# Kernel tuning notes

Hardware: AMD Instinct MI355X
Metric: run time of the kernel (lower is better)

## Reference

```python
import jax, jax.numpy as jnp
import numpy as np

# Multi-scale deformable attention (Deformable-DETR / MMCV MSDA), faithful math.
SHAPES = [(100, 100), (50, 50), (25, 25), (13, 13)]  # (H_l, W_l) per level
B, C, NH, L, P = 2, 256, 8, 4, 4
LV = sum(h * w for h, w in SHAPES)  # 13294
LQ = LV
D = C // NH  # head dim = 32


def setup_inputs() -> dict:
    k = jax.random.split(jax.random.key(0), 10)
    rn = lambda i, sh, sc=1.0: jax.random.normal(k[i], sh, jnp.float32) * sc
    starts = np.cumsum([0] + [h * w for h, w in SHAPES])[:L]
    return {
        "query": rn(0, (LQ, B, C)),
        "reference_points": jax.random.uniform(k[1], (B, LQ, L, 2), jnp.float32),
        "value": rn(2, (LV, B, C)),
        "spatial_shapes": jnp.array(SHAPES, jnp.int32),
        "level_start_index": jnp.array(starts, jnp.int32),
        "Wv": rn(3, (C, C), C ** -0.5), "bv": jnp.zeros((C,), jnp.float32),
        "Woff": rn(4, (C, NH * L * P * 2), 0.01), "boff": rn(5, (NH * L * P * 2,), 0.3),
        "Wattn": rn(6, (C, NH * L * P), 0.02), "battn": jnp.zeros((NH * L * P,), jnp.float32),
        "Wo": rn(7, (C, C), C ** -0.5), "bo": jnp.zeros((C,), jnp.float32),
    }


def _bilinear(v, loc, Hl, Wl):
    """v: [B,NH,Hl*Wl,D]; loc: [B,Lq,NH,P,2] normalized (x,y) in (0,1).
    grid_sample(align_corners=False, padding_mode='zeros') equivalent."""
    x = loc[..., 0] * Wl - 0.5
    y = loc[..., 1] * Hl - 0.5
    x0 = jnp.floor(x); y0 = jnp.floor(y)
    wx = x - x0; wy = y - y0
    x0i = x0.astype(jnp.int32); y0i = y0.astype(jnp.int32)
    lq = loc.shape[1]
    acc = jnp.zeros((B, NH, lq * P, D), v.dtype)
    for dy, wyc in ((0, 1.0 - wy), (1, wy)):
        for dx, wxc in ((0, 1.0 - wx), (1, wx)):
            xi = x0i + dx; yi = y0i + dy
            valid = (xi >= 0) & (xi < Wl) & (yi >= 0) & (yi < Hl)
            idx = jnp.clip(yi, 0, Hl - 1) * Wl + jnp.clip(xi, 0, Wl - 1)  # [B,Lq,NH,P]
            idx2 = jnp.transpose(idx, (0, 2, 1, 3)).reshape(B, NH, lq * P)
            g = jnp.take_along_axis(v, idx2[..., None], axis=2)  # [B,NH,Lq*P,D]
            w = jnp.where(valid, wyc * wxc, 0.0).astype(v.dtype)
            w2 = jnp.transpose(w, (0, 2, 1, 3)).reshape(B, NH, lq * P, 1)
            acc = acc + g * w2
    return acc.reshape(B, NH, lq, P, D)


def _msda(q, rp, v, spatial_shapes, Wv, bv, Woff, boff, Wattn, battn, Wo, bo):
    # q: [B,Lq,C], v: [B,Lv,C] (batch-first), rp: [B,Lq,L,2]
    rp = jnp.clip(rp, 1e-5, 1.0 - 1e-5)  # wrapper clamp
    val = (v @ Wv + bv).reshape(B, LV, NH, D)
    val = jnp.transpose(val, (0, 2, 1, 3))  # [B,NH,Lv,D]
    off = (q @ Woff + boff).reshape(B, LQ, NH, L, P, 2)
    attn = jax.nn.softmax((q @ Wattn + battn).reshape(B, LQ, NH, L * P), axis=-1)
    attn = attn.reshape(B, LQ, NH, L, P)
    ss = spatial_shapes.astype(jnp.float32)
    norm = jnp.stack([ss[:, 1], ss[:, 0]], -1)  # [L,2] = (W_l, H_l)
    loc = rp[:, :, None, :, None, :] + off / norm[None, None, None, :, None, :]
    out = jnp.zeros((B, LQ, NH, D), q.dtype)
    start = 0
    for lvl, (Hl, Wl) in enumerate(SHAPES):
        vl = val[:, :, start:start + Hl * Wl]  # [B,NH,Hl*Wl,D]
        sampled = _bilinear(vl, loc[:, :, :, lvl], Hl, Wl)  # [B,NH,Lq,P,D]
        out = out + jnp.einsum('bhqpd,bqhp->bqhd', sampled, attn[:, :, :, lvl])
        start += Hl * Wl
    out = out.reshape(B, LQ, C) @ Wo + bo
    return out + q  # MMCV residual: dropout(output) + identity (dropout=0 at eval)


def reference(query, reference_points, value, spatial_shapes, level_start_index,
              Wv, bv, Woff, boff, Wattn, battn, Wo, bo):
    q = jnp.swapaxes(query, 0, 1)   # wrapper: seq-first -> batch-first
    v = jnp.swapaxes(value, 0, 1)
    out = _msda(q, reference_points, v, spatial_shapes,
                Wv, bv, Woff, boff, Wattn, battn, Wo, bo)
    return jnp.swapaxes(out, 0, 1)  # back to [Lq,B,C]
```

## Files before the change

kernel.cpp:

```cpp
#include <hip/hip_runtime.h>
#include <math.h>

namespace {

typedef __attribute__((ext_vector_type(8))) short short8;
typedef __attribute__((ext_vector_type(4))) float f32x4;
typedef __attribute__((ext_vector_type(2))) float f32x2;

constexpr int B  = 2;
constexpr int C  = 256;
constexpr int NH = 8;
constexpr int L  = 4;
constexpr int P  = 4;
constexpr int D  = 32;
constexpr int LV = 13294;
constexpr int LQ = 13294;
constexpr int M  = B * LQ;

constexpr int SZ[4]    = {100, 50, 25, 13};
constexpr int START[4] = {0, 10000, 12500, 13125};

__device__ inline short bf16r(float f) {
  unsigned u = __float_as_uint(f);
  u += 0x7fff + ((u >> 16) & 1);
  return (short)(u >> 16);
}

__device__ inline short8 cvt8(const f32x4 lo, const f32x4 hi) {
  union { uint4 u; short8 s; } r;
  asm("v_cvt_pk_bf16_f32 %0, %1, %2" : "=v"(r.u.x) : "v"(lo[0]), "v"(lo[1]));
  asm("v_cvt_pk_bf16_f32 %0, %1, %2" : "=v"(r.u.y) : "v"(lo[2]), "v"(lo[3]));
  asm("v_cvt_pk_bf16_f32 %0, %1, %2" : "=v"(r.u.z) : "v"(hi[0]), "v"(hi[1]));
  asm("v_cvt_pk_bf16_f32 %0, %1, %2" : "=v"(r.u.w) : "v"(hi[2]), "v"(hi[3]));
  return r.s;
}

__device__ inline void load_a_cvt(const float* __restrict__ arow, short8 a[8]) {
#pragma unroll
  for (int s = 0; s < 8; ++s) {
    const f32x4 lo = *reinterpret_cast<const f32x4*>(arow + s * 32);
    const f32x4 hi = *reinterpret_cast<const f32x4*>(arow + s * 32 + 4);
    a[s] = cvt8(lo, hi);
  }
}

__device__ inline void load_a_bf16(const unsigned short* __restrict__ arow, short8 a[8]) {
#pragma unroll
  for (int s = 0; s < 8; ++s)
    a[s] = *reinterpret_cast<const short8*>(arow + s * 32);
}

__device__ inline void glds16(const unsigned short* g, unsigned short* l) {
  __builtin_amdgcn_global_load_lds(
      (const __attribute__((address_space(1))) void*)g,
      (__attribute__((address_space(3))) void*)l, 16, 0, 0);
}

__global__ __launch_bounds__(256) void k_pre(
    const float* __restrict__ Wv, const float* __restrict__ Woff,
    const float* __restrict__ Wattn, const float* __restrict__ Wo,
    unsigned short* __restrict__ Btv, unsigned short* __restrict__ Btoa,
    unsigned short* __restrict__ Bto) {
  __shared__ float tile[32][33];
  const int blk = blockIdx.x;
  const float* src; unsigned short* dst; int N, local;
  if (blk < 64)       { src = Wv;    dst = Btv;              N = 256; local = blk; }
  else if (blk < 128) { src = Woff;  dst = Btoa;             N = 256; local = blk - 64; }
  else if (blk < 160) { src = Wattn; dst = Btoa + 256 * 256; N = 128; local = blk - 128; }
  else                { src = Wo;    dst = Bto;              N = 256; local = blk - 160; }
  const int ntiles = N >> 5;
  const int kt = local / ntiles, nt = local - kt * ntiles;
  const int k0 = kt << 5, n0 = nt << 5;
  const int tx = threadIdx.x & 31, ty = threadIdx.x >> 5;
#pragma unroll
  for (int r = 0; r < 4; ++r) {
    const int kk = ty + r * 8;
    tile[kk][tx] = src[(size_t)(k0 + kk) * N + n0 + tx];
  }
  __syncthreads();
#pragma unroll
  for (int r = 0; r < 4; ++r) {
    const int nn = ty + r * 8;
    const int n = n0 + nn, k = k0 + tx;
    dst[(size_t)n * 256 + (k ^ ((n & 7) << 3))] = (unsigned short)bf16r(tile[tx][nn]);
  }
}

__global__ __launch_bounds__(256, 4) void k_gemm12(
    const float* __restrict__ query, const float* __restrict__ value,
    const float* __restrict__ rp,
    const unsigned short* __restrict__ Btv, const unsigned short* __restrict__ Btoa,
    const float* __restrict__ bv, const float* __restrict__ boff,
    const float* __restrict__ battn,
    unsigned short* __restrict__ val, float* __restrict__ loc,
    float* __restrict__ attn) {
  __shared__ unsigned short sB[64 * 256];
  __shared__ float sRP[64][9];
  const int tid = threadIdx.x;
  const int wave = tid >> 6, lane = tid & 63, quad = lane >> 4, lo = lane & 15;
  const bool isval = (blockIdx.y == 0);
  const float* __restrict__ Af = isval ? value : query;
  const unsigned short* Bt  = isval ? Btv : Btoa;
  const int NC = isval ? 4 : 6;
  const int m0 = blockIdx.x * 64;
  const int mrow = m0 + wave * 16;

  short8 a[8];
  {
    const int mr = min(mrow + lo, M - 1);
    const int bb = mr / LQ, ii = mr - bb * LQ;
    load_a_cvt(Af + ((size_t)(ii * 2 + bb)) * 256 + quad * 8, a);
  }

  if (!isval && tid < 128) {
    const int r = tid >> 1, q4 = (tid & 1) * 4;
    const int mr = min(m0 + r, M - 1);
    f32x4 v = *reinterpret_cast<const f32x4*>(rp + (size_t)mr * 8 + q4);
#pragma unroll
    for (int j = 0; j < 4; ++j) v[j] = fminf(fmaxf(v[j], 1e-5f), 1.f - 1e-5f);
    *reinterpret_cast<f32x4*>(&sRP[r][q4]) = v;
  }

  const int sw = lo & 7;

#pragma unroll 1
  for (int ch = 0; ch < NC; ++ch) {
    const int n0 = ch * 64;
    __syncthreads();
    {
      const unsigned short* gsrc = Bt + (size_t)n0 * 256 + wave * 4096 + lane * 8;
      unsigned short* lbase = &sB[wave * 4096];
#pragma unroll
      for (int i = 0; i < 8; ++i)
        glds16(gsrc + i * 512, lbase + i * 512);
    }
    __syncthreads();

#pragma unroll 1
    for (int tt = 0; tt < 4; ++tt) {
      const unsigned short* bbase = &sB[(tt * 16 + lo) * 256];
      short8 b[8];
#pragma unroll
      for (int s = 0; s < 8; ++s)
        b[s] = *reinterpret_cast<const short8*>(bbase + (((quad + s * 4) ^ sw) << 3));
      f32x4 acc = (f32x4){0.f, 0.f, 0.f, 0.f};
#pragma unroll
      for (int s = 0; s < 8; ++s)
        acc = __builtin_amdgcn_mfma_f32_16x16x32_bf16(b[s], a[s], acc, 0, 0, 0);

      const int nb = n0 + tt * 16 + quad * 4;
      const int m = mrow + lo;
      if (isval) {
        const f32x4 bias4 = *reinterpret_cast<const f32x4*>(bv + nb);
        const int h = nb >> 5, d0 = nb & 31;
        if (m < M) {
          const int bb = m / LV, i = m - bb * LV;
          ushort4 o;
          o.x = (unsigned short)bf16r(acc[0] + bias4[0]);
          o.y = (unsigned short)bf16r(acc[1] + bias4[1]);
          o.z = (unsigned short)bf16r(acc[2] + bias4[2]);
          o.w = (unsigned short)bf16r(acc[3] + bias4[3]);
          *reinterpret_cast<ushort4*>(
              val + (((size_t)(bb * NH + h)) * LV + i) * D + d0) = o;
        }
      } else if (ch < 4) {
        const f32x4 bias4 = *reinterpret_cast<const f32x4*>(boff + nb);
        const int l = (nb >> 3) & 3;
        const float rsz = (l == 0) ? 0.01f : (l == 1) ? 0.02f
                        : (l == 2) ? 0.04f : (1.f / 13.f);
        if (m < M) {
          const int lr = wave * 16 + lo;
          const float rx = sRP[lr][l * 2];
          const float ry = sRP[lr][l * 2 + 1];
          f32x4 o;
          o[0] = fmaf(acc[0] + bias4[0], rsz, rx);
          o[1] = fmaf(acc[1] + bias4[1], rsz, ry);
          o[2] = fmaf(acc[2] + bias4[2], rsz, rx);
          o[3] = fmaf(acc[3] + bias4[3], rsz, ry);
          *reinterpret_cast<f32x4*>(loc + (size_t)m * 256 + nb) = o;
        }
      } else {
        const int n2 = nb - 256;
        const f32x4 bias4 = *reinterpret_cast<const f32x4*>(battn + n2);
        float v0 = acc[0] + bias4[0], v1 = acc[1] + bias4[1];
        float v2 = acc[2] + bias4[2], v3 = acc[3] + bias4[3];
        float mx = fmaxf(fmaxf(v0, v1), fmaxf(v2, v3));
        mx = fmaxf(mx, __shfl_xor(mx, 16, 64));
        mx = fmaxf(mx, __shfl_xor(mx, 32, 64));
        const float e0 = __expf(v0 - mx), e1 = __expf(v1 - mx);
        const float e2 = __expf(v2 - mx), e3 = __expf(v3 - mx);
        float s = e0 + e1 + e2 + e3;
        s += __shfl_xor(s, 16, 64);
        s += __shfl_xor(s, 32, 64);
        const float inv = 1.f / s;
        if (m < M) {
          f32x4 o; o[0] = e0 * inv; o[1] = e1 * inv; o[2] = e2 * inv; o[3] = e3 * inv;
          *reinterpret_cast<f32x4*>(attn + (size_t)m * 128 + n2) = o;
        }
      }
    }
  }
}

__global__ __launch_bounds__(256, 4) void k_gemm3(
    const unsigned short* __restrict__ tmp, const float* __restrict__ query,
    const unsigned short* __restrict__ Bt, const float* __restrict__ bo,
    float* __restrict__ out) {
  __shared__ unsigned short sB[64 * 256];
  const int tid = threadIdx.x;
  const int wave = tid >> 6, lane = tid & 63, quad = lane >> 4, lo = lane & 15;
  const int m0 = blockIdx.x * 64;
  const int mrow = m0 + wave * 16;

  short8 a[8];
  {
    const int mr = min(mrow + lo, M - 1);
    load_a_bf16(tmp + (size_t)mr * 256 + quad * 8, a);
  }
  const int sw = lo & 7;

#pragma unroll 1
  for (int ch = 0; ch < 4; ++ch) {
    const int n0 = ch * 64;
    __syncthreads();
    {
      const unsigned short* gsrc = Bt + (size_t)n0 * 256 + wave * 4096 + lane * 8;
      unsigned short* lbase = &sB[wave * 4096];
#pragma unroll
      for (int i = 0; i < 8; ++i)
        glds16(gsrc + i * 512, lbase + i * 512);
    }
    __syncthreads();

#pragma unroll 1
    for (int tt = 0; tt < 4; ++tt) {
      const unsigned short* bbase = &sB[(tt * 16 + lo) * 256];
      short8 b[8];
#pragma unroll
      for (int s = 0; s < 8; ++s)
        b[s] = *reinterpret_cast<const short8*>(bbase + (((quad + s * 4) ^ sw) << 3));
      f32x4 acc = (f32x4){0.f, 0.f, 0.f, 0.f};
#pragma unroll
      for (int s = 0; s < 8; ++s)
        acc = __builtin_amdgcn_mfma_f32_16x16x32_bf16(b[s], a[s], acc, 0, 0, 0);
      const int nb = n0 + tt * 16 + quad * 4;
      const f32x4 bias4 = *reinterpret_cast<const f32x4*>(bo + nb);
      const int m = mrow + lo;
      if (m < M) {
        const int bb = m / LQ, q = m - bb * LQ;
        const size_t o = ((size_t)(q * B + bb)) * C + nb;
        const f32x4 qv = *reinterpret_cast<const f32x4*>(query + o);
        f32x4 ov;
        ov[0] = acc[0] + bias4[0] + qv[0];
        ov[1] = acc[1] + bias4[1] + qv[1];
        ov[2] = acc[2] + bias4[2] + qv[2];
        ov[3] = acc[3] + bias4[3] + qv[3];
        *reinterpret_cast<f32x4*>(out + o) = ov;
      }
    }
  }
}

#define QB_I(v, PAT) __builtin_amdgcn_ds_swizzle((v), (PAT))
#define QB_F(v, PAT) __int_as_float(__builtin_amdgcn_ds_swizzle(__float_as_int(v), (PAT)))

__device__ inline void msda_corner(f32x2 acc[4], const uint4 r, const float w) {
  const f32x2 wv = {w, w};
  f32x2 v;
  v[0] = __uint_as_float(r.x << 16);
  v[1] = __uint_as_float(r.x & 0xffff0000u);
  acc[0] = __builtin_elementwise_fma(v, wv, acc[0]);
  v[0] = __uint_as_float(r.y << 16);
  v[1] = __uint_as_float(r.y & 0xffff0000u);
  acc[1] = __builtin_elementwise_fma(v, wv, acc[1]);
  v[0] = __uint_as_float(r.z << 16);
  v[1] = __uint_as_float(r.z & 0xffff0000u);
  acc[2] = __builtin_elementwise_fma(v, wv, acc[2]);
  v[0] = __uint_as_float(r.w << 16);
  v[1] = __uint_as_float(r.w & 0xffff0000u);
  acc[3] = __builtin_elementwise_fma(v, wv, acc[3]);
}

__global__ __launch_bounds__(256, 4) void k_sample(
    const unsigned short* __restrict__ val, const float* __restrict__ loc,
    const float* __restrict__ attn, unsigned short* __restrict__ tmp) {
  constexpr int QPB = 8;
  const int mblk = blockIdx.x * QPB;
  const int t = threadIdx.x;
  __shared__ float sloc[QPB * 8 * 33];
  __shared__ float sattn[QPB * 8 * 17];
  for (int i = t; i < QPB * 256; i += 256) {
    int mq = mblk + (i >> 8); if (mq >= M) mq = M - 1;
    const int j = i & 255;
    sloc[(((i >> 8) << 3) + (j >> 5)) * 33 + (j & 31)] = loc[(size_t)mq * 256 + j];
  }
  for (int i = t; i < QPB * 128; i += 256) {
    int mq = mblk + (i >> 7); if (mq >= M) mq = M - 1;
    const int j = i & 127;
    sattn[(((i >> 7) << 3) + (j >> 4)) * 17 + (j & 15)] = attn[(size_t)mq * 128 + j];
  }
  __syncthreads();

  const int g = t >> 5, s = t & 31, h = s >> 2, c8 = s & 3;
  const int m = mblk + g;
  const int mc = (m < M) ? m : M - 1;
  const int b = mc / LQ;
  const unsigned short* vhead = val + ((size_t)(b * NH + h) * LV) * D + c8 * 8;
  const float* ql = sloc + (g * 8 + h) * 33;
  const float* qa = sattn + (g * 8 + h) * 17;

  f32x2 acc[4];
  acc[0] = (f32x2){0.f, 0.f}; acc[1] = (f32x2){0.f, 0.f};
  acc[2] = (f32x2){0.f, 0.f}; acc[3] = (f32x2){0.f, 0.f};
#pragma unroll 1
  for (int l = 0; l < L; ++l) {
    const int Wl = SZ[l];
    const float Wlf = (float)Wl;
    const unsigned short* vlev = vhead + (size_t)START[l] * D;
    const float x = ql[l * 8 + c8 * 2]     * Wlf - 0.5f;
    const float y = ql[l * 8 + c8 * 2 + 1] * Wlf - 0.5f;
    const float aw = qa[l * 4 + c8];
    const float x0f = floorf(x), y0f = floorf(y);
    const float wx = x - x0f, wy = y - y0f;
    const int x0 = (int)x0f, y0 = (int)y0f;
    const int x1 = x0 + 1, y1 = y0 + 1;
    const float wy1v = wy * aw;
    const float wy0m = ((unsigned)y0 < (unsigned)Wl) ? (aw - wy1v) : 0.f;
    const float wy1m = ((unsigned)y1 < (unsigned)Wl) ? wy1v : 0.f;
    const float wx0m = ((unsigned)x0 < (unsigned)Wl) ? (1.f - wx) : 0.f;
    const float wx1m = ((unsigned)x1 < (unsigned)Wl) ? wx : 0.f;
    const int xc0 = min(max(x0, 0), Wl - 1), xc1 = min(max(x1, 0), Wl - 1);
    const int yc0 = min(max(y0, 0), Wl - 1), yc1 = min(max(y1, 0), Wl - 1);
    const int r0 = yc0 * Wl, r1 = yc1 * Wl;
    const int o00 = (r0 + xc0) * D, o01 = (r0 + xc1) * D;
    const int o10 = (r1 + xc0) * D, o11 = (r1 + xc1) * D;
    const float w00 = wy0m * wx0m, w01 = wy0m * wx1m;
    const float w10 = wy1m * wx0m, w11 = wy1m * wx1m;

    int   off[16];
    float ww[16];
#define MSDA_BCAST(P, PAT)                                                \
    off[(P)*4+0] = QB_I(o00, PAT); off[(P)*4+1] = QB_I(o01, PAT);         \
    off[(P)*4+2] = QB_I(o10, PAT); off[(P)*4+3] = QB_I(o11, PAT);         \
    ww[(P)*4+0]  = QB_F(w00, PAT); ww[(P)*4+1]  = QB_F(w01, PAT);         \
    ww[(P)*4+2]  = QB_F(w10, PAT); ww[(P)*4+3]  = QB_F(w11, PAT);
    MSDA_BCAST(0, 0x8000)
    MSDA_BCAST(1, 0x8055)
    MSDA_BCAST(2, 0x80AA)
    MSDA_BCAST(3, 0x80FF)
#undef MSDA_BCAST

    uint4 v[16];
#pragma unroll
    for (int i = 0; i < 16; ++i)
      v[i] = *reinterpret_cast<const uint4*>(vlev + off[i]);

#pragma unroll
    for (int i = 0; i < 16; ++i)
      msda_corner(acc, v[i], ww[i]);
  }
  if (m < M) {
    short8 o;
#pragma unroll
    for (int j = 0; j < 4; ++j) {
      o[2 * j]     = bf16r(acc[j][0]);
      o[2 * j + 1] = bf16r(acc[j][1]);
    }
    *reinterpret_cast<short8*>(tmp + (size_t)m * 256 + h * 32 + c8 * 8) = o;
  }
}

}

extern "C" void kernel_launch(void* const* d_in, const int* in_sizes, int n_in,
                              void* d_out, int out_size, void* d_ws, size_t ws_size,
                              hipStream_t stream) {
  const float* query = (const float*)d_in[0];
  const float* rp    = (const float*)d_in[1];
  const float* value = (const float*)d_in[2];
  const float* Wv    = (const float*)d_in[5];
  const float* bv    = (const float*)d_in[6];
  const float* Woff  = (const float*)d_in[7];
  const float* boff  = (const float*)d_in[8];
  const float* Wattn = (const float*)d_in[9];
  const float* battn = (const float*)d_in[10];
  const float* Wo    = (const float*)d_in[11];
  const float* bo    = (const float*)d_in[12];
  float* out = (float*)d_out;

  unsigned short* Btv  = (unsigned short*)d_ws;
  unsigned short* Btoa = Btv + 256 * 256;
  unsigned short* Bto  = Btoa + 384 * 256;
  unsigned short* val  = Bto + 256 * 256;
  float* loc  = (float*)(val + (size_t)M * 256);
  float* attn = loc + (size_t)M * 256;
  unsigned short* tmp = (unsigned short*)(attn + (size_t)M * 128);

  const int mtiles64 = (M + 63) / 64;
  const int sample_blocks = (M + 7) / 8;

  k_pre<<<224, 256, 0, stream>>>(Wv, Woff, Wattn, Wo, Btv, Btoa, Bto);
  k_gemm12<<<dim3(mtiles64, 2), 256, 0, stream>>>(query, value, rp, Btv, Btoa,
                                                  bv, boff, battn, val, loc, attn);
  k_sample<<<sample_blocks, 256, 0, stream>>>(val, loc, attn, tmp);
  k_gemm3<<<mtiles64, 256, 0, stream>>>(tmp, query, Bto, bo, out);
}
```

Measured before the change: 203.6 us.

## Fuse output projection GEMM into deformable sampling kernel via LDS staging

The sampling kernel now writes its bf16 per-query results into shared memory and immediately runs the output projection with MFMA. It also adds the bias and query residual before writing the final output. This removes the separate gemm3 launch and the global round trip of the intermediate tmp buffer. In exchange, each 8-query block reloads the full Wo matrix from global/L2 and wastes half of each 16-row MFMA tile on duplicated rows.

After: 217.3 us. +6.7%, slower.

```diff
diff --git a/kernel.cpp b/kernel.cpp
--- a/kernel.cpp
+++ b/kernel.cpp
@@ -42,12 +42,6 @@
     const f32x4 hi = *reinterpret_cast<const f32x4*>(arow + s * 32 + 4);
     a[s] = cvt8(lo, hi);
   }
-}
-
-__device__ inline void load_a_bf16(const unsigned short* __restrict__ arow, short8 a[8]) {
-#pragma unroll
-  for (int s = 0; s < 8; ++s)
-    a[s] = *reinterpret_cast<const short8*>(arow + s * 32);
 }
 
 __device__ inline void glds16(const unsigned short* g, unsigned short* l) {
@@ -202,65 +196,6 @@
   }
 }
 
-__global__ __launch_bounds__(256, 4) void k_gemm3(
-    const unsigned short* __restrict__ tmp, const float* __restrict__ query,
-    const unsigned short* __restrict__ Bt, const float* __restrict__ bo,
-    float* __restrict__ out) {
-  __shared__ unsigned short sB[64 * 256];
-  const int tid = threadIdx.x;
-  const int wave = tid >> 6, lane = tid & 63, quad = lane >> 4, lo = lane & 15;
-  const int m0 = blockIdx.x * 64;
-  const int mrow = m0 + wave * 16;
-
-  short8 a[8];
-  {
-    const int mr = min(mrow + lo, M - 1);
-    load_a_bf16(tmp + (size_t)mr * 256 + quad * 8, a);
-  }
-  const int sw = lo & 7;
-
-#pragma unroll 1
-  for (int ch = 0; ch < 4; ++ch) {
-    const int n0 = ch * 64;
-    __syncthreads();
-    {
-      const unsigned short* gsrc = Bt + (size_t)n0 * 256 + wave * 4096 + lane * 8;
-      unsigned short* lbase = &sB[wave * 4096];
-#pragma unroll
-      for (int i = 0; i < 8; ++i)
-        glds16(gsrc + i * 512, lbase + i * 512);
-    }
-    __syncthreads();
-
-#pragma unroll 1
-    for (int tt = 0; tt < 4; ++tt) {
-      const unsigned short* bbase = &sB[(tt * 16 + lo) * 256];
-      short8 b[8];
-#pragma unroll
-      for (int s = 0; s < 8; ++s)
-        b[s] = *reinterpret_cast<const short8*>(bbase + (((quad + s * 4) ^ sw) << 3));
-      f32x4 acc = (f32x4){0.f, 0.f, 0.f, 0.f};
-#pragma unroll
-      for (int s = 0; s < 8; ++s)
-        acc = __builtin_amdgcn_mfma_f32_16x16x32_bf16(b[s], a[s], acc, 0, 0, 0);
-      const int nb = n0 + tt * 16 + quad * 4;
-      const f32x4 bias4 = *reinterpret_cast<const f32x4*>(bo + nb);
-      const int m = mrow + lo;
-      if (m < M) {
-        const int bb = m / LQ, q = m - bb * LQ;
-        const size_t o = ((size_t)(q * B + bb)) * C + nb;
-        const f32x4 qv = *reinterpret_cast<const f32x4*>(query + o);
-        f32x4 ov;
-        ov[0] = acc[0] + bias4[0] + qv[0];
-        ov[1] = acc[1] + bias4[1] + qv[1];
-        ov[2] = acc[2] + bias4[2] + qv[2];
-        ov[3] = acc[3] + bias4[3] + qv[3];
-        *reinterpret_cast<f32x4*>(out + o) = ov;
-      }
-    }
-  }
-}
-
 #define QB_I(v, PAT) __builtin_amdgcn_ds_swizzle((v), (PAT))
 #define QB_F(v, PAT) __int_as_float(__builtin_amdgcn_ds_swizzle(__float_as_int(v), (PAT)))
 
@@ -283,12 +218,15 @@
 
 __global__ __launch_bounds__(256, 4) void k_sample(
     const unsigned short* __restrict__ val, const float* __restrict__ loc,
-    const float* __restrict__ attn, unsigned short* __restrict__ tmp) {
+    const float* __restrict__ attn, const unsigned short* __restrict__ Bto,
+    const float* __restrict__ query, const float* __restrict__ bo,
+    float* __restrict__ out) {
   constexpr int QPB = 8;
   const int mblk = blockIdx.x * QPB;
   const int t = threadIdx.x;
   __shared__ float sloc[QPB * 8 * 33];
   __shared__ float sattn[QPB * 8 * 17];
+  __shared__ unsigned short stmp[QPB * 264];
   for (int i = t; i < QPB * 256; i += 256) {
     int mq = mblk + (i >> 8); if (mq >= M) mq = M - 1;
     const int j = i & 255;
@@ -359,14 +297,51 @@
     for (int i = 0; i < 16; ++i)
       msda_corner(acc, v[i], ww[i]);
   }
-  if (m < M) {
+  {
     short8 o;
 #pragma unroll
     for (int j = 0; j < 4; ++j) {
       o[2 * j]     = bf16r(acc[j][0]);
       o[2 * j + 1] = bf16r(acc[j][1]);
     }
-    *reinterpret_cast<short8*>(tmp + (size_t)m * 256 + h * 32 + c8 * 8) = o;
+    *reinterpret_cast<short8*>(stmp + g * 264 + h * 32 + c8 * 8) = o;
+  }
+  __syncthreads();
+
+  const int wave = t >> 6, lane = t & 63, quad = lane >> 4, lo = lane & 15;
+  short8 a2[8];
+#pragma unroll
+  for (int s2 = 0; s2 < 8; ++s2)
+    a2[s2] = *reinterpret_cast<const short8*>(
+        stmp + (lo & 7) * 264 + quad * 8 + s2 * 32);
+
+#pragma unroll 1
+  for (int ct = 0; ct < 4; ++ct) {
+    const int n0 = ct * 64 + wave * 16;
+    const unsigned short* bsrc = Bto + (size_t)(n0 + lo) * 256;
+    short8 bb[8];
+#pragma unroll
+    for (int s2 = 0; s2 < 8; ++s2)
+      bb[s2] = *reinterpret_cast<const short8*>(
+          bsrc + (((quad + s2 * 4) ^ (lo & 7)) << 3));
+    f32x4 acc2 = (f32x4){0.f, 0.f, 0.f, 0.f};
+#pragma unroll
+    for (int s2 = 0; s2 < 8; ++s2)
+      acc2 = __builtin_amdgcn_mfma_f32_16x16x32_bf16(bb[s2], a2[s2], acc2, 0, 0, 0);
+    const int nb = n0 + quad * 4;
+    const f32x4 bias4 = *reinterpret_cast<const f32x4*>(bo + nb);
+    const int mo = mblk + lo;
+    if (lo < 8 && mo < M) {
+      const int b2 = mo / LQ, q = mo - b2 * LQ;
+      const size_t o = ((size_t)(q * B + b2)) * C + nb;
+      const f32x4 qv = *reinterpret_cast<const f32x4*>(query + o);
+      f32x4 ov;
+      ov[0] = acc2[0] + bias4[0] + qv[0];
+      ov[1] = acc2[1] + bias4[1] + qv[1];
+      ov[2] = acc2[2] + bias4[2] + qv[2];
+      ov[3] = acc2[3] + bias4[3] + qv[3];
+      *reinterpret_cast<f32x4*>(out + o) = ov;
+    }
   }
 }
 
@@ -394,7 +369,6 @@
   unsigned short* val  = Bto + 256 * 256;
   float* loc  = (float*)(val + (size_t)M * 256);
   float* attn = loc + (size_t)M * 256;
-  unsigned short* tmp = (unsigned short*)(attn + (size_t)M * 128);
 
   const int mtiles64 = (M + 63) / 64;
   const int sample_blocks = (M + 7) / 8;
@@ -402,6 +376,5 @@
   k_pre<<<224, 256, 0, stream>>>(Wv, Woff, Wattn, Wo, Btv, Btoa, Bto);
   k_gemm12<<<dim3(mtiles64, 2), 256, 0, stream>>>(query, value, rp, Btv, Btoa,
                                                   bv, boff, battn, val, loc, attn);
-  k_sample<<<sample_blocks, 256, 0, stream>>>(val, loc, attn, tmp);
-  k_gemm3<<<mtiles64, 256, 0, stream>>>(tmp, query, Bto, bo, out);
-}
+  k_sample<<<sample_blocks, 256, 0, stream>>>(val, loc, attn, Bto, query, bo, out);
+}
```

## Double-buffer LDS weight tiles in projection GEMMs with 32-column chunks

Applied to the files above, without the earlier changes.

Both projection GEMM kernels now split the weight matrix into 32-column chunks held in two LDS buffers. The next chunk is prefetched asynchronously while the current one is consumed, which leaves one barrier per chunk instead of two. The inner tile loop is also fully unrolled. This aims to hide global-to-LDS latency behind the MFMA work, at the cost of twice as many loop iterations and reliance on the barrier draining the outstanding async loads.

Measured after the change: 203.8 us. Within noise of the previous version (+0.1%).

```diff
diff --git a/kernel.cpp b/kernel.cpp
--- a/kernel.cpp
+++ b/kernel.cpp
@@ -94,20 +94,21 @@
     const float* __restrict__ battn,
     unsigned short* __restrict__ val, float* __restrict__ loc,
     float* __restrict__ attn) {
-  __shared__ unsigned short sB[64 * 256];
+  __shared__ unsigned short sB[2][32 * 256];
   __shared__ float sRP[64][9];
   const int tid = threadIdx.x;
   const int wave = tid >> 6, lane = tid & 63, quad = lane >> 4, lo = lane & 15;
   const bool isval = (blockIdx.y == 0);
   const float* __restrict__ Af = isval ? value : query;
   const unsigned short* Bt  = isval ? Btv : Btoa;
-  const int NC = isval ? 4 : 6;
+  const int NC = isval ? 8 : 12;
   const int m0 = blockIdx.x * 64;
   const int mrow = m0 + wave * 16;
+  const int m = mrow + lo;
 
   short8 a[8];
   {
-    const int mr = min(mrow + lo, M - 1);
+    const int mr = min(m, M - 1);
     const int bb = mr / LQ, ii = mr - bb * LQ;
     load_a_cvt(Af + ((size_t)(ii * 2 + bb)) * 256 + quad * 8, a);
   }
@@ -123,22 +124,26 @@
 
   const int sw = lo & 7;
 
+#define STAGE14(BUF, CH)                                                    \
+  {                                                                         \
+    const unsigned short* gsrc = Bt + (size_t)(CH) * 8192 + wave * 2048 + lane * 8; \
+    unsigned short* lbase = &sB[(BUF)][wave * 2048];                        \
+    glds16(gsrc,        lbase);                                             \
+    glds16(gsrc + 512,  lbase + 512);                                       \
+    glds16(gsrc + 1024, lbase + 1024);                                      \
+    glds16(gsrc + 1536, lbase + 1536);                                      \
+  }
+
+  STAGE14(0, 0)
+  int cur = 0;
 #pragma unroll 1
   for (int ch = 0; ch < NC; ++ch) {
-    const int n0 = ch * 64;
     __syncthreads();
-    {
-      const unsigned short* gsrc = Bt + (size_t)n0 * 256 + wave * 4096 + lane * 8;
-      unsigned short* lbase = &sB[wave * 4096];
-#pragma unroll
-      for (int i = 0; i < 8; ++i)
-        glds16(gsrc + i * 512, lbase + i * 512);
-    }
-    __syncthreads();
-
-#pragma unroll 1
-    for (int tt = 0; tt < 4; ++tt) {
-      const unsigned short* bbase = &sB[(tt * 16 + lo) * 256];
+    if (ch + 1 < NC) STAGE14(cur ^ 1, ch + 1)
+
+#pragma unroll
+    for (int tt = 0; tt < 2; ++tt) {
+      const unsigned short* bbase = &sB[cur][(tt * 16 + lo) * 256];
       short8 b[8];
 #pragma unroll
       for (int s = 0; s < 8; ++s)
@@ -148,8 +153,7 @@
       for (int s = 0; s < 8; ++s)
         acc = __builtin_amdgcn_mfma_f32_16x16x32_bf16(b[s], a[s], acc, 0, 0, 0);
 
-      const int nb = n0 + tt * 16 + quad * 4;
-      const int m = mrow + lo;
+      const int nb = ch * 32 + tt * 16 + quad * 4;
       if (isval) {
         const f32x4 bias4 = *reinterpret_cast<const f32x4*>(bv + nb);
         const int h = nb >> 5, d0 = nb & 31;
@@ -163,7 +167,7 @@
           *reinterpret_cast<ushort4*>(
               val + (((size_t)(bb * NH + h)) * LV + i) * D + d0) = o;
         }
-      } else if (ch < 4) {
+      } else if (ch < 8) {
         const f32x4 bias4 = *reinterpret_cast<const f32x4*>(boff + nb);
         const int l = (nb >> 3) & 3;
         const float rsz = (l == 0) ? 0.01f : (l == 1) ? 0.02f
@@ -199,6 +203,7 @@
         }
       }
     }
+    cur ^= 1;
   }
 }
 
@@ -206,35 +211,30 @@
     const unsigned short* __restrict__ tmp, const float* __restrict__ query,
     const unsigned short* __restrict__ Bt, const float* __restrict__ bo,
     float* __restrict__ out) {
-  __shared__ unsigned short sB[64 * 256];
+  __shared__ unsigned short sB[2][32 * 256];
   const int tid = threadIdx.x;
   const int wave = tid >> 6, lane = tid & 63, quad = lane >> 4, lo = lane & 15;
   const int m0 = blockIdx.x * 64;
   const int mrow = m0 + wave * 16;
+  const int m = mrow + lo;
 
   short8 a[8];
   {
-    const int mr = min(mrow + lo, M - 1);
+    const int mr = min(m, M - 1);
     load_a_bf16(tmp + (size_t)mr * 256 + quad * 8, a);
   }
   const int sw = lo & 7;
 
+  STAGE14(0, 0)
+  int cur = 0;
 #pragma unroll 1
-  for (int ch = 0; ch < 4; ++ch) {
-    const int n0 = ch * 64;
+  for (int ch = 0; ch < 8; ++ch) {
     __syncthreads();
-    {
-      const unsigned short* gsrc = Bt + (size_t)n0 * 256 + wave * 4096 + lane * 8;
-      unsigned short* lbase = &sB[wave * 4096];
-#pragma unroll
-      for (int i = 0; i < 8; ++i)
-        glds16(gsrc + i * 512, lbase + i * 512);
-    }
-    __syncthreads();
-
-#pragma unroll 1
-    for (int tt = 0; tt < 4; ++tt) {
-      const unsigned short* bbase = &sB[(tt * 16 + lo) * 256];
+    if (ch + 1 < 8) STAGE14(cur ^ 1, ch + 1)
+
+#pragma unroll
+    for (int tt = 0; tt < 2; ++tt) {
+      const unsigned short* bbase = &sB[cur][(tt * 16 + lo) * 256];
       short8 b[8];
 #pragma unroll
       for (int s = 0; s < 8; ++s)
@@ -243,9 +243,8 @@
 #pragma unroll
       for (int s = 0; s < 8; ++s)
         acc = __builtin_amdgcn_mfma_f32_16x16x32_bf16(b[s], a[s], acc, 0, 0, 0);
-      const int nb = n0 + tt * 16 + quad * 4;
+      const int nb = ch * 32 + tt * 16 + quad * 4;
       const f32x4 bias4 = *reinterpret_cast<const f32x4*>(bo + nb);
-      const int m = mrow + lo;
       if (m < M) {
         const int bb = m / LQ, q = m - bb * LQ;
         const size_t o = ((size_t)(q * B + bb)) * C + nb;
@@ -258,8 +257,10 @@
         *reinterpret_cast<f32x4*>(out + o) = ov;
       }
     }
-  }
-}
+    cur ^= 1;
+  }
+}
+#undef STAGE14
 
 #define QB_I(v, PAT) __builtin_amdgcn_ds_swizzle((v), (PAT))
 #define QB_F(v, PAT) __int_as_float(__builtin_amdgcn_ds_swizzle(__float_as_int(v), (PAT)))
```
